# Kernel tuning notes

Measured on AMD Instinct MI355X. Metric: run time of the kernel, lower is better.

## Reference

```python
import jax, jax.numpy as jnp
import numpy as np
import math

NUM_HEADS = 16


def setup_inputs() -> dict:
    key = jax.random.key(0)
    ks = jax.random.split(key, 6)
    L, B, E = 1024, 4, 1024
    D = E // NUM_HEADS
    return {
        "query": jax.random.normal(ks[0], (L, B, E), dtype=jnp.float32),
        "relpos_mat": jax.random.normal(ks[1], (L, D), dtype=jnp.float32),
        "in_proj_weight": jax.random.normal(ks[2], (3 * E, E), dtype=jnp.float32) * 0.02,
        "in_proj_bias": jax.random.normal(ks[3], (3 * E,), dtype=jnp.float32) * 0.02,
        "out_proj_weight": jax.random.normal(ks[4], (E, E), dtype=jnp.float32) * 0.02,
        "out_proj_bias": jax.random.normal(ks[5], (E,), dtype=jnp.float32) * 0.02,
    }


def _skew(qe):
    # qe: (B*H, L, L). Music-Transformer skew trick.
    sz = qe.shape[1]
    mask = jnp.flip(jnp.triu(jnp.ones((sz, sz), dtype=qe.dtype)), axis=0)
    qe = qe * mask
    qe = jnp.pad(qe, ((0, 0), (0, 0), (1, 0)))  # (BH, L, L+1)
    qe = qe.reshape(qe.shape[0], sz + 1, sz)     # (BH, L+1, L)
    return qe[:, 1:, :]                          # (BH, L, L)


def reference(query, relpos_mat, in_proj_weight, in_proj_bias, out_proj_weight, out_proj_bias):
    L, B, E = query.shape
    H = NUM_HEADS
    D = E // H

    # packed QKV projection (self-attention path)
    qkv = query @ in_proj_weight.T + in_proj_bias  # (L, B, 3E)
    q, k, v = jnp.split(qkv, 3, axis=-1)

    def to_bh(x):  # (L, B, E) -> (B*H, L, D)
        return x.reshape(L, B * H, D).transpose(1, 0, 2)

    q = to_bh(q) / math.sqrt(D)
    k = to_bh(k)
    v = to_bh(v)

    attn = jnp.einsum('bld,bmd->blm', q, k)  # (BH, L, L)

    # valid relative embeddings: last L rows
    start = max(0, relpos_mat.shape[0] - L)
    er = relpos_mat[start:, :]               # (L, D)
    qe = jnp.einsum('hld,md->hlm', q, er)    # (BH, L, L)
    srel = _skew(qe)

    attn = jax.nn.softmax(attn + srel, axis=-1)
    out = jnp.einsum('blm,bmd->bld', attn, v)            # (BH, L, D)
    out = out.transpose(1, 0, 2).reshape(L, B, E)         # (L, B, E)
    out = out @ out_proj_weight.T + out_proj_bias
    return out
```

## Files before the change

kernel.cpp:

```cpp
#include <hip/hip_runtime.h>
#include <hip/hip_bf16.h>

#define SL 1024
#define BB 4
#define EE 1024
#define HH 16
#define DD 64
#define BHC 64
#define M1 4096

typedef __bf16 bf16x8 __attribute__((ext_vector_type(8)));
typedef __bf16 bf16x4 __attribute__((ext_vector_type(4)));
typedef float f32x4 __attribute__((ext_vector_type(4)));

typedef __attribute__((address_space(3))) unsigned int lds_u32;
typedef const __attribute__((address_space(1))) unsigned int g_u32;

__device__ __forceinline__ f32x4 mfma16(bf16x8 a, bf16x8 b, f32x4 c) {
    return __builtin_amdgcn_mfma_f32_16x16x32_bf16(a, b, c, 0, 0, 0);
}

#define FR(buf, row, chunk) (*(const bf16x8*)&(buf)[(row) * 64 + (((chunk) ^ ((row) & 7))) * 8])

__global__ __launch_bounds__(256) void f32_to_bf16_k(const float* __restrict__ in,
                                                     __bf16* __restrict__ out, int n) {
    int idx = (blockIdx.x * 256 + threadIdx.x) * 4;
    if (idx >= n) return;
    float4 v = *(const float4*)&in[idx];
    bf16x4 o;
    o[0] = (__bf16)v.x; o[1] = (__bf16)v.y; o[2] = (__bf16)v.z; o[3] = (__bf16)v.w;
    *(bf16x4*)&out[idx] = o;
}

__global__ __launch_bounds__(256) void erflip_k(const float* __restrict__ rel,
                                                __bf16* __restrict__ erf) {
    int idx = blockIdx.x * 256 + threadIdx.x;
    int r = idx >> 6, d = idx & 63;
    erf[idx] = (__bf16)rel[(1023 - r) * 64 + d];
}

#define BMt 128
#define BNt 128
#define BKt 32
__global__ __launch_bounds__(256) void gemm_bt(const __bf16* __restrict__ A,
                                               const __bf16* __restrict__ Bm,
                                               const float* __restrict__ bias,
                                               int M, int N, int K, int mode,
                                               __bf16* __restrict__ q_ws,
                                               __bf16* __restrict__ k_ws,
                                               __bf16* __restrict__ vT_ws,
                                               float* __restrict__ outf) {
    __shared__ __bf16 As[BMt * BKt];
    __shared__ __bf16 Bs[BNt * BKt];
    int tid = threadIdx.x;
    int wave = tid >> 6, lane = tid & 63;
    int quad = lane >> 4, c = lane & 15;
    int ntiles = N / BNt;
    int bx = blockIdx.x % ntiles, by = blockIdx.x / ntiles;
    int m0 = by * BMt, n0 = bx * BNt;
    int wm = (wave >> 1) * 64, wn = (wave & 1) * 64;
    int srow = lane >> 2, scol = (lane & 3) * 8;

    f32x4 acc[4][4] = {};
    for (int k0 = 0; k0 < K; k0 += BKt) {
        __syncthreads();
#pragma unroll
        for (int n = 0; n < 2; ++n) {
            int r0 = 32 * wave + 16 * n;
            const __bf16* ga = &A[(long)(m0 + r0 + srow) * K + k0 + scol];
            const __bf16* gb = &Bm[(long)(n0 + r0 + srow) * K + k0 + scol];
            __builtin_amdgcn_global_load_lds((g_u32*)ga, (lds_u32*)&As[r0 * BKt], 16, 0, 0);
            __builtin_amdgcn_global_load_lds((g_u32*)gb, (lds_u32*)&Bs[r0 * BKt], 16, 0, 0);
        }
        __syncthreads();
        bf16x8 af[4], bfr[4];
#pragma unroll
        for (int t = 0; t < 4; ++t) {
            af[t]  = *(const bf16x8*)&As[(wm + t * 16 + c) * BKt + quad * 8];
            bfr[t] = *(const bf16x8*)&Bs[(wn + t * 16 + c) * BKt + quad * 8];
        }
#pragma unroll
        for (int mt = 0; mt < 4; ++mt)
#pragma unroll
            for (int nt = 0; nt < 4; ++nt)
                acc[mt][nt] = mfma16(af[mt], bfr[nt], acc[mt][nt]);
    }

    if (mode == 1) {
#pragma unroll
        for (int mt = 0; mt < 4; ++mt)
#pragma unroll
            for (int nt = 0; nt < 4; ++nt) {
                int nn = n0 + wn + nt * 16 + c;
                float bv = bias[nn];
#pragma unroll
                for (int i = 0; i < 4; ++i) {
                    int mm = m0 + wm + mt * 16 + quad * 4 + i;
                    outf[(long)mm * N + nn] = acc[mt][nt][i] + bv;
                }
            }
        return;
    }
    __syncthreads();
    __bf16* slab = ((wave < 2) ? As : Bs) + (wave & 1) * 2048;
    int nnb = n0 + wn;
    int which = nnb >> 10;
    int hh = (nnb & 1023) >> 6;
    float scale = (which == 0) ? 0.125f : 1.0f;
#pragma unroll
    for (int mt = 0; mt < 4; ++mt) {
#pragma unroll
        for (int nt = 0; nt < 4; ++nt) {
            float bv = bias[nnb + nt * 16 + c];
#pragma unroll
            for (int i = 0; i < 4; ++i)
                slab[(quad * 4 + i) * 72 + nt * 16 + c] =
                    (__bf16)((acc[mt][nt][i] + bv) * scale);
        }
        if (which < 2) {
            int mm = m0 + wm + mt * 16 + c;
            int l = mm >> 2, bb = mm & 3;
            __bf16* dstp = ((which == 0) ? q_ws : k_ws) +
                           ((long)(bb * 16 + hh) * 1024 + l) * 64;
            bf16x8 t0 = *(const bf16x8*)&slab[c * 72 + quad * 8];
            bf16x8 t1 = *(const bf16x8*)&slab[c * 72 + 32 + quad * 8];
            *(bf16x8*)&dstp[quad * 8] = t0;
            *(bf16x8*)&dstp[32 + quad * 8] = t1;
        } else {
            int d = quad * 16 + c;
            __bf16 tmp[16];
#pragma unroll
            for (int jr = 0; jr < 16; ++jr) tmp[jr] = slab[jr * 72 + d];
            int L0 = (m0 + wm + mt * 16) >> 2;
#pragma unroll
            for (int bs = 0; bs < 4; ++bs) {
                bf16x4 pk;
                pk[0] = tmp[bs]; pk[1] = tmp[4 + bs];
                pk[2] = tmp[8 + bs]; pk[3] = tmp[12 + bs];
                *(bf16x4*)&vT_ws[((long)(bs * 16 + hh) * 64 + d) * 1024 + L0] = pk;
            }
        }
    }
}

#define RSTn 72
__global__ __launch_bounds__(256, 2) void attn_kernel(const __bf16* __restrict__ q_ws,
                                                      const __bf16* __restrict__ k_ws,
                                                      const __bf16* __restrict__ vT_ws,
                                                      const __bf16* __restrict__ erf,
                                                      __bf16* __restrict__ O_flat) {
    __shared__ __bf16 Ks[2][4096];
    __shared__ __bf16 Vs[4096];
    __shared__ __bf16 Es[2][4096];
    __shared__ __bf16 Ring[4][2][32 * RSTn];

    int tid = threadIdx.x;
    int w = tid >> 6, lane = tid & 63;
    int q = lane >> 4, c = lane & 15;
    int bid = blockIdx.x;
    int x = bid & 7, ii = bid >> 3;
    int bh = x * 8 + (ii >> 3);
    int blk_l0 = (ii & 7) * 128;
    int b = bh >> 4, h = bh & 15;
    int l0w = blk_l0 + w * 32;

    __bf16* RW = &Ring[w][0][0];

    const __bf16* qp = q_ws + ((long)bh * 1024 + l0w) * 64;
    bf16x8 qf0[2], qf1[2];
    qf0[0] = *(const bf16x8*)&qp[c * 64 + q * 8];
    qf1[0] = *(const bf16x8*)&qp[c * 64 + 32 + q * 8];
    qf0[1] = *(const bf16x8*)&qp[(16 + c) * 64 + q * 8];
    qf1[1] = *(const bf16x8*)&qp[(16 + c) * 64 + 32 + q * 8];

    const __bf16* kbase = k_ws + (long)bh * 65536;
    const __bf16* vbase = vT_ws + (long)bh * 65536;

    int sr[2], sc[2], ldo[2];
#pragma unroll
    for (int n = 0; n < 2; ++n) {
        int sidx = w * 128 + n * 64 + lane;
        sr[n] = sidx >> 3;
        sc[n] = (sidx & 7) ^ (sr[n] & 7);
        ldo[n] = (w * 128 + n * 64) * 8;
    }

#pragma unroll
    for (int n = 0; n < 2; ++n)
        __builtin_amdgcn_global_load_lds((g_u32*)(kbase + 15 * 4096 + sr[n] * 64 + sc[n] * 8),
                                         (lds_u32*)&Ks[1][ldo[n]], 16, 0, 0);
    __syncthreads();

    f32x4 O[2][4] = {};
    float l_run[2] = {0.f, 0.f};

    for (int kt = 15; kt >= 0; --kt) {
        int p = kt & 1;
        if (kt > 0) {
#pragma unroll
            for (int n = 0; n < 2; ++n)
                __builtin_amdgcn_global_load_lds(
                    (g_u32*)(kbase + (kt - 1) * 4096 + sr[n] * 64 + sc[n] * 8),
                    (lds_u32*)&Ks[p ^ 1][ldo[n]], 16, 0, 0);
        }
#pragma unroll
        for (int n = 0; n < 2; ++n)
            __builtin_amdgcn_global_load_lds(
                (g_u32*)(vbase + sr[n] * 1024 + kt * 64 + sc[n] * 8),
                (lds_u32*)&Vs[ldo[n]], 16, 0, 0);
        int rmaxB = blk_l0 + 127 - kt * 64;
        if (rmaxB >= 0) {
            int tB = rmaxB >> 6;
#pragma unroll
            for (int n = 0; n < 2; ++n)
                __builtin_amdgcn_global_load_lds(
                    (g_u32*)(erf + tB * 4096 + sr[n] * 64 + sc[n] * 8),
                    (lds_u32*)&Es[tB & 1][ldo[n]], 16, 0, 0);
        }
        const __bf16* Kp = Ks[p];
        bf16x8 ka0[4], ka1[4];
#pragma unroll
        for (int s = 0; s < 4; ++s) {
            int row = 16 * s + c;
            ka0[s] = FR(Kp, row, q);
            ka1[s] = FR(Kp, row, 4 + q);
        }
        f32x4 S[2][4];
#pragma unroll
        for (int g = 0; g < 2; ++g)
#pragma unroll
            for (int s = 0; s < 4; ++s) {
                f32x4 acc = {0.f, 0.f, 0.f, 0.f};
                acc = mfma16(ka0[s], qf0[g], acc);
                acc = mfma16(ka1[s], qf1[g], acc);
                S[g][s] = acc;
            }
        __syncthreads();
        int rmax = l0w + 31 - kt * 64;
        int t1 = rmax >> 6;
        if (rmax >= 0) {
            const __bf16* Ep = Es[t1 & 1];
            bf16x8 ea0[4], ea1[4];
#pragma unroll
            for (int s = 0; s < 4; ++s) {
                int row = 16 * s + c;
                ea0[s] = FR(Ep, row, q);
                ea1[s] = FR(Ep, row, 4 + q);
            }
            __bf16* rt = RW + (t1 & 1) * 2304;
#pragma unroll
            for (int g = 0; g < 2; ++g)
#pragma unroll
                for (int s = 0; s < 4; ++s) {
                    f32x4 ar = {0.f, 0.f, 0.f, 0.f};
                    ar = mfma16(ea0[s], qf0[g], ar);
                    ar = mfma16(ea1[s], qf1[g], ar);
                    bf16x4 pk;
#pragma unroll
                    for (int i = 0; i < 4; ++i) pk[i] = (__bf16)ar[i];
                    *(bf16x4*)&rt[(g * 16 + c) * RSTn + 16 * s + 4 * q] = pk;
                }
#pragma unroll
            for (int g = 0; g < 2; ++g) {
                int rb = l0w + g * 16 + c - kt * 64 - 4 * q;
#pragma unroll
                for (int s = 0; s < 4; ++s)
#pragma unroll
                    for (int i = 0; i < 4; ++i) {
                        int r = rb - 16 * s - i;
                        if (r >= 0)
                            S[g][s][i] += (float)RW[((r >> 6) & 1) * 2304 +
                                                    (g * 16 + c) * RSTn + (r & 63)];
                    }
            }
        }
        int pslot = (rmax >= 0) ? ((t1 & 1) ^ 1) : 1;
#pragma unroll
        for (int g = 0; g < 2; ++g) {
            float ps[4];
#pragma unroll
            for (int s = 0; s < 4; ++s) {
                float a = __expf(S[g][s][0]), b2 = __expf(S[g][s][1]);
                float c2 = __expf(S[g][s][2]), d2 = __expf(S[g][s][3]);
                S[g][s][0] = a; S[g][s][1] = b2; S[g][s][2] = c2; S[g][s][3] = d2;
                ps[s] = (a + b2) + (c2 + d2);
            }
            l_run[g] += (ps[0] + ps[1]) + (ps[2] + ps[3]);
        }
        __bf16* PW = RW + pslot * 2304;
#pragma unroll
        for (int g = 0; g < 2; ++g)
#pragma unroll
            for (int s = 0; s < 4; ++s) {
                bf16x4 pk;
#pragma unroll
                for (int i = 0; i < 4; ++i) pk[i] = (__bf16)S[g][s][i];
                *(bf16x4*)&PW[(g * 16 + c) * RSTn + 16 * s + 4 * q] = pk;
            }
        bf16x8 va0[4], va1[4];
#pragma unroll
        for (int s = 0; s < 4; ++s) {
            int row = 16 * s + c;
            va0[s] = FR(Vs, row, q);
            va1[s] = FR(Vs, row, 4 + q);
        }
        bf16x8 pa0[2], pa1[2];
#pragma unroll
        for (int g = 0; g < 2; ++g) {
            pa0[g] = *(const bf16x8*)&PW[(g * 16 + c) * RSTn + q * 8];
            pa1[g] = *(const bf16x8*)&PW[(g * 16 + c) * RSTn + 32 + q * 8];
        }
#pragma unroll
        for (int g = 0; g < 2; ++g)
#pragma unroll
            for (int s = 0; s < 4; ++s) {
                O[g][s] = mfma16(va0[s], pa0[g], O[g][s]);
                O[g][s] = mfma16(va1[s], pa1[g], O[g][s]);
            }
        __syncthreads();
    }
#pragma unroll
    for (int g = 0; g < 2; ++g) {
        float tot = l_run[g];
        tot += __shfl_xor(tot, 16);
        tot += __shfl_xor(tot, 32);
        float rs = 1.0f / tot;
        long row = (long)(l0w + g * 16 + c) * 4 + b;
#pragma unroll
        for (int s = 0; s < 4; ++s) {
            bf16x4 ov;
#pragma unroll
            for (int i = 0; i < 4; ++i) ov[i] = (__bf16)(O[g][s][i] * rs);
            *(bf16x4*)&O_flat[row * 1024 + h * 64 + 16 * s + 4 * q] = ov;
        }
    }
}

extern "C" void kernel_launch(void* const* d_in, const int* in_sizes, int n_in,
                              void* d_out, int out_size, void* d_ws, size_t ws_size,
                              hipStream_t stream) {
    const float* query  = (const float*)d_in[0];
    const float* relpos = (const float*)d_in[1];
    const float* w_in   = (const float*)d_in[2];
    const float* b_in   = (const float*)d_in[3];
    const float* w_out  = (const float*)d_in[4];
    const float* b_out  = (const float*)d_in[5];
    float* out = (float*)d_out;

    char* ws = (char*)d_ws;
    size_t off = 0;
    auto alloc = [&](size_t bytes) {
        void* p = ws + off;
        off += (bytes + 255) & ~(size_t)255;
        return p;
    };
    __bf16* qA    = (__bf16*)alloc((size_t)M1 * EE * 2);
    __bf16* winb  = (__bf16*)alloc((size_t)3 * EE * EE * 2);
    __bf16* woutb = (__bf16*)alloc((size_t)EE * EE * 2);
    __bf16* erfp  = (__bf16*)alloc((size_t)SL * DD * 2);
    __bf16* q_ws  = (__bf16*)alloc((size_t)BHC * SL * DD * 2);
    __bf16* k_ws  = (__bf16*)alloc((size_t)BHC * SL * DD * 2);
    __bf16* vT_ws = (__bf16*)alloc((size_t)BHC * SL * DD * 2);
    __bf16* O_flat= (__bf16*)alloc((size_t)M1 * EE * 2);

    f32_to_bf16_k<<<4096, 256, 0, stream>>>(query, qA, M1 * EE);
    f32_to_bf16_k<<<3072, 256, 0, stream>>>(w_in, winb, 3 * EE * EE);
    f32_to_bf16_k<<<1024, 256, 0, stream>>>(w_out, woutb, EE * EE);
    erflip_k<<<256, 256, 0, stream>>>(relpos, erfp);

    gemm_bt<<<(3072 / BNt) * (M1 / BMt), 256, 0, stream>>>(
        qA, winb, b_in, M1, 3072, EE, 0, q_ws, k_ws, vT_ws, nullptr);

    attn_kernel<<<512, 256, 0, stream>>>(q_ws, k_ws, vT_ws, erfp, O_flat);

    gemm_bt<<<(1024 / BNt) * (M1 / BMt), 256, 0, stream>>>(
        O_flat, woutb, b_out, M1, 1024, EE, 1, nullptr, nullptr, nullptr, out);
}
```

Baseline: 216.1 us.

## Double-buffer V, read relpos fragments from global, and fuse prep kernels

```diff
diff --git a/kernel.cpp b/kernel.cpp
--- a/kernel.cpp
+++ b/kernel.cpp
@@ -22,21 +22,34 @@
 
 #define FR(buf, row, chunk) (*(const bf16x8*)&(buf)[(row) * 64 + (((chunk) ^ ((row) & 7))) * 8])
 
-__global__ __launch_bounds__(256) void f32_to_bf16_k(const float* __restrict__ in,
-                                                     __bf16* __restrict__ out, int n) {
-    int idx = (blockIdx.x * 256 + threadIdx.x) * 4;
-    if (idx >= n) return;
-    float4 v = *(const float4*)&in[idx];
+__global__ __launch_bounds__(256) void prep_k(const float* __restrict__ query,
+                                              const float* __restrict__ w_in,
+                                              const float* __restrict__ w_out,
+                                              const float* __restrict__ rel,
+                                              __bf16* __restrict__ qA,
+                                              __bf16* __restrict__ winb,
+                                              __bf16* __restrict__ woutb,
+                                              __bf16* __restrict__ erfp) {
+    int bid = blockIdx.x, tid = threadIdx.x;
+    const float* src;
+    __bf16* dst;
+    int idx;
+    if (bid < 4096)      { src = query; dst = qA;    idx = (bid * 256 + tid) * 4; }
+    else if (bid < 7168) { src = w_in;  dst = winb;  idx = ((bid - 4096) * 256 + tid) * 4; }
+    else if (bid < 8192) { src = w_out; dst = woutb; idx = ((bid - 7168) * 256 + tid) * 4; }
+    else {
+        int e4 = ((bid - 8192) * 256 + tid) * 4;
+        int r = e4 >> 6, d = e4 & 63;
+        float4 v = *(const float4*)&rel[(1023 - r) * 64 + d];
+        bf16x4 o;
+        o[0] = (__bf16)v.x; o[1] = (__bf16)v.y; o[2] = (__bf16)v.z; o[3] = (__bf16)v.w;
+        *(bf16x4*)&erfp[e4] = o;
+        return;
+    }
+    float4 v = *(const float4*)&src[idx];
     bf16x4 o;
     o[0] = (__bf16)v.x; o[1] = (__bf16)v.y; o[2] = (__bf16)v.z; o[3] = (__bf16)v.w;
-    *(bf16x4*)&out[idx] = o;
-}
-
-__global__ __launch_bounds__(256) void erflip_k(const float* __restrict__ rel,
-                                                __bf16* __restrict__ erf) {
-    int idx = blockIdx.x * 256 + threadIdx.x;
-    int r = idx >> 6, d = idx & 63;
-    erf[idx] = (__bf16)rel[(1023 - r) * 64 + d];
+    *(bf16x4*)&dst[idx] = o;
 }
 
 #define BMt 128
@@ -144,15 +157,15 @@
 }
 
 #define RSTn 72
+#define RSLOT (32 * RSTn)
 __global__ __launch_bounds__(256, 2) void attn_kernel(const __bf16* __restrict__ q_ws,
                                                       const __bf16* __restrict__ k_ws,
                                                       const __bf16* __restrict__ vT_ws,
                                                       const __bf16* __restrict__ erf,
                                                       __bf16* __restrict__ O_flat) {
     __shared__ __bf16 Ks[2][4096];
-    __shared__ __bf16 Vs[4096];
-    __shared__ __bf16 Es[2][4096];
-    __shared__ __bf16 Ring[4][2][32 * RSTn];
+    __shared__ __bf16 Vs[2][4096];
+    __shared__ __bf16 Ring[4][2][RSLOT];
 
     int tid = threadIdx.x;
     int w = tid >> 6, lane = tid & 63;
@@ -186,9 +199,12 @@
     }
 
 #pragma unroll
-    for (int n = 0; n < 2; ++n)
+    for (int n = 0; n < 2; ++n) {
         __builtin_amdgcn_global_load_lds((g_u32*)(kbase + 15 * 4096 + sr[n] * 64 + sc[n] * 8),
                                          (lds_u32*)&Ks[1][ldo[n]], 16, 0, 0);
+        __builtin_amdgcn_global_load_lds((g_u32*)(vbase + sr[n] * 1024 + 15 * 64 + sc[n] * 8),
+                                         (lds_u32*)&Vs[1][ldo[n]], 16, 0, 0);
+    }
     __syncthreads();
 
     f32x4 O[2][4] = {};
@@ -198,24 +214,25 @@
         int p = kt & 1;
         if (kt > 0) {
 #pragma unroll
-            for (int n = 0; n < 2; ++n)
+            for (int n = 0; n < 2; ++n) {
                 __builtin_amdgcn_global_load_lds(
                     (g_u32*)(kbase + (kt - 1) * 4096 + sr[n] * 64 + sc[n] * 8),
                     (lds_u32*)&Ks[p ^ 1][ldo[n]], 16, 0, 0);
-        }
-#pragma unroll
-        for (int n = 0; n < 2; ++n)
-            __builtin_amdgcn_global_load_lds(
-                (g_u32*)(vbase + sr[n] * 1024 + kt * 64 + sc[n] * 8),
-                (lds_u32*)&Vs[ldo[n]], 16, 0, 0);
-        int rmaxB = blk_l0 + 127 - kt * 64;
-        if (rmaxB >= 0) {
-            int tB = rmaxB >> 6;
-#pragma unroll
-            for (int n = 0; n < 2; ++n)
                 __builtin_amdgcn_global_load_lds(
-                    (g_u32*)(erf + tB * 4096 + sr[n] * 64 + sc[n] * 8),
-                    (lds_u32*)&Es[tB & 1][ldo[n]], 16, 0, 0);
+                    (g_u32*)(vbase + sr[n] * 1024 + (kt - 1) * 64 + sc[n] * 8),
+                    (lds_u32*)&Vs[p ^ 1][ldo[n]], 16, 0, 0);
+            }
+        }
+        int rmax = l0w + 31 - kt * 64;
+        int t1 = rmax >> 6;
+        bf16x8 ea0[4], ea1[4];
+        if (rmax >= 0) {
+            const __bf16* ep = erf + (long)t1 * 4096;
+#pragma unroll
+            for (int s = 0; s < 4; ++s) {
+                ea0[s] = *(const bf16x8*)&ep[(16 * s + c) * 64 + q * 8];
+                ea1[s] = *(const bf16x8*)&ep[(16 * s + c) * 64 + 32 + q * 8];
+            }
         }
         const __bf16* Kp = Ks[p];
         bf16x8 ka0[4], ka1[4];
@@ -235,19 +252,8 @@
                 acc = mfma16(ka1[s], qf1[g], acc);
                 S[g][s] = acc;
             }
-        __syncthreads();
-        int rmax = l0w + 31 - kt * 64;
-        int t1 = rmax >> 6;
         if (rmax >= 0) {
-            const __bf16* Ep = Es[t1 & 1];
-            bf16x8 ea0[4], ea1[4];
-#pragma unroll
-            for (int s = 0; s < 4; ++s) {
-                int row = 16 * s + c;
-                ea0[s] = FR(Ep, row, q);
-                ea1[s] = FR(Ep, row, 4 + q);
-            }
-            __bf16* rt = RW + (t1 & 1) * 2304;
+            __bf16* rt = RW + (t1 & 1) * RSLOT;
 #pragma unroll
             for (int g = 0; g < 2; ++g)
 #pragma unroll
@@ -269,7 +275,7 @@
                     for (int i = 0; i < 4; ++i) {
                         int r = rb - 16 * s - i;
                         if (r >= 0)
-                            S[g][s][i] += (float)RW[((r >> 6) & 1) * 2304 +
+                            S[g][s][i] += (float)RW[((r >> 6) & 1) * RSLOT +
                                                     (g * 16 + c) * RSTn + (r & 63)];
                     }
             }
@@ -287,7 +293,7 @@
             }
             l_run[g] += (ps[0] + ps[1]) + (ps[2] + ps[3]);
         }
-        __bf16* PW = RW + pslot * 2304;
+        __bf16* PW = RW + pslot * RSLOT;
 #pragma unroll
         for (int g = 0; g < 2; ++g)
 #pragma unroll
@@ -297,12 +303,13 @@
                 for (int i = 0; i < 4; ++i) pk[i] = (__bf16)S[g][s][i];
                 *(bf16x4*)&PW[(g * 16 + c) * RSTn + 16 * s + 4 * q] = pk;
             }
+        const __bf16* Vp = Vs[p];
         bf16x8 va0[4], va1[4];
 #pragma unroll
         for (int s = 0; s < 4; ++s) {
             int row = 16 * s + c;
-            va0[s] = FR(Vs, row, q);
-            va1[s] = FR(Vs, row, 4 + q);
+            va0[s] = FR(Vp, row, q);
+            va1[s] = FR(Vp, row, 4 + q);
         }
         bf16x8 pa0[2], pa1[2];
 #pragma unroll
@@ -363,10 +370,8 @@
     __bf16* vT_ws = (__bf16*)alloc((size_t)BHC * SL * DD * 2);
     __bf16* O_flat= (__bf16*)alloc((size_t)M1 * EE * 2);
 
-    f32_to_bf16_k<<<4096, 256, 0, stream>>>(query, qA, M1 * EE);
-    f32_to_bf16_k<<<3072, 256, 0, stream>>>(w_in, winb, 3 * EE * EE);
-    f32_to_bf16_k<<<1024, 256, 0, stream>>>(w_out, woutb, EE * EE);
-    erflip_k<<<256, 256, 0, stream>>>(relpos, erfp);
+    prep_k<<<8256, 256, 0, stream>>>(query, w_in, w_out, relpos,
+                                     qA, winb, woutb, erfp);
 
     gemm_bt<<<(3072 / BNt) * (M1 / BMt), 256, 0, stream>>>(
         qA, winb, b_in, M1, 3072, EE, 0, q_ws, k_ws, vT_ws, nullptr);
```

Result: slower. 221.3 us (+2.4%).
